# Optimization experiments

Hardware: AMD Instinct MI355X
Metric: run time of the kernel (lower is better)

## Reference

```python
import jax, jax.numpy as jnp
import numpy as np

B, N, D = 32768, 20, 13  # batch, n_humans, rotated-state dim (last input channel is mask)
LAYERS = {
    'm1': [(D, 150), (150, 100)],          # mlp1, last_relu=True
    'm2': [(100, 100), (100, 50)],          # mlp2
    'at': [(200, 100), (100, 100), (100, 1)],  # attention (global state concat -> 2*100 in)
    'hp': [(100, 100), (100, 100), (100, 7)],  # human_state_predictor (50*2 in)
}

def _mlp(x, params, last_relu=False):
    n = len(params)
    for i, (W, b) in enumerate(params):
        x = x @ W + b
        if i < n - 1 or last_relu:
            x = jax.nn.relu(x)
    return x

def setup_inputs() -> dict:
    key = jax.random.key(0)
    ks, kx, km = jax.random.split(key, 3)
    inp = {}
    for name, shapes in LAYERS.items():
        for i, (fi, fo) in enumerate(shapes):
            kw, kb, ks = jax.random.split(jax.random.fold_in(ks, i), 3)
            inp[f'{name}_w{i}'] = jax.random.normal(kw, (fi, fo), jnp.float32) / jnp.sqrt(float(fi))
            inp[f'{name}_b{i}'] = jnp.zeros((fo,), jnp.float32)
    x = jax.random.normal(kx, (B, N, D + 1), jnp.float32)
    mask = (jax.random.uniform(km, (B, N)) < 0.9).astype(jnp.float32)  # 0/1 visibility mask
    inp['state'] = x.at[..., -1].set(mask)
    return inp

def reference(state, m1_w0, m1_b0, m1_w1, m1_b1,
              m2_w0, m2_b0, m2_w1, m2_b1,
              at_w0, at_b0, at_w1, at_b1, at_w2, at_b2,
              hp_w0, hp_b0, hp_w1, hp_b1, hp_w2, hp_b2):
    x, mask = state[..., :-1], state[..., -1]        # (B,N,D), (B,N)
    h1 = _mlp(x, [(m1_w0, m1_b0), (m1_w1, m1_b1)], last_relu=True)   # (B,N,100)
    h2 = _mlp(h1, [(m2_w0, m2_b0), (m2_w1, m2_b1)])                   # (B,N,50)

    # masked mean-pool global state (NaN-on-empty zeroed, as in torch)
    msum = jnp.sum(mask, axis=1, keepdims=True)                       # (B,1)
    mw = jnp.where(msum > 0, mask / jnp.where(msum > 0, msum, 1.0), 0.0)
    global_state = jnp.sum(mw[..., None] * h1, axis=1, keepdims=True) # (B,1,100)
    att_in = jnp.concatenate([h1, jnp.broadcast_to(global_state, h1.shape)], axis=-1)

    scores = _mlp(att_in, [(at_w0, at_b0), (at_w1, at_b1), (at_w2, at_b2)])[..., 0]  # (B,N)
    scores = scores * mask
    se = jnp.exp(scores) * (scores != 0).astype(scores.dtype)
    ssum = jnp.sum(se, axis=1, keepdims=True)
    w = jnp.where(ssum > 0, se / jnp.where(ssum > 0, ssum, 1.0), 0.0)[..., None]  # (B,N,1)

    wsum = jnp.sum(w * h2, axis=1, keepdims=True)                     # (B,1,50)
    joint = jnp.concatenate([h2, jnp.broadcast_to(wsum, h2.shape)], axis=-1)  # (B,N,100)
    return _mlp(joint, [(hp_w0, hp_b0), (hp_w1, hp_b1), (hp_w2, hp_b2)])      # (B,N,7)
```

## Files before the change

### kernel.cpp

```cpp
#include <hip/hip_runtime.h>


typedef short sx8 __attribute__((ext_vector_type(8)));
typedef short sx4 __attribute__((ext_vector_type(4)));
typedef float fx4 __attribute__((ext_vector_type(4)));

#define TB   512
#define NW   8
#define NB   4
#define MTOK 80
#define MT   5
#define CHH  640
#define CHG  128

#define OFF_BUFT 0
#define OFF_BUFA 25600
#define OFF_BUFH 46080
#define OFF_BUFG 56320
#define OFF_BIAS 60416
#define OFF_GRC  63808
#define OFF_WRC  65408
#define OFF_SC   67008
#define OFF_MASK 67328
#define OFF_MSUM 67648
#define OFF_SSUM 67664
#define SMEM_BYTES 67680

#define B_M1B0 0
#define B_M1B1 152
#define B_M2B0 256
#define B_M2B1 360
#define B_ATB0 416
#define B_ATB1 520
#define B_HPB0 624
#define B_HPB1 728
#define B_HPB2 832

#define WS_M1W0  0
#define WS_M1W1  5120
#define WS_M2W0  23040
#define WS_M2W1  37376
#define WS_ATW0  45568
#define WS_ATW1  59904
#define WS_HPW0  74240
#define WS_HPW1  81408
#define WS_HPW2  95744
#define WS_ATW0H 97792
#define WS_HPW0H 112128

__device__ __forceinline__ short f2b(float f) {
    unsigned u = __builtin_bit_cast(unsigned, f);
    u += 0x7FFFu + ((u >> 16) & 1u);
    return (short)(u >> 16);
}
__device__ __forceinline__ float b2f(short h) {
    unsigned u = ((unsigned)(unsigned short)h) << 16;
    return __builtin_bit_cast(float, u);
}

__device__ __forceinline__ void stg(const float* __restrict__ W, int N,
                                    int KR, int KPAD, int NR, int Nsrc,
                                    short* dst, int gtid, int gsz) {
    int K8 = KPAD >> 3;
    for (int idx = gtid; idx < NR * K8; idx += gsz) {
        int k8 = idx / NR, nl = idx - k8 * NR;
        int k0 = k8 << 3;
        sx8 h;
        #pragma unroll
        for (int i = 0; i < 8; ++i) {
            int k = k0 + i;
            float v = (k < KR && nl < Nsrc) ? W[k * N + nl] : 0.f;
            h[i] = f2b(v);
        }
        *(sx8*)(dst + (k8 * NR + nl) * 8) = h;
    }
}

__global__ void stage_weights(
    const float* __restrict__ m1w0, const float* __restrict__ m1w1,
    const float* __restrict__ m2w0, const float* __restrict__ m2w1,
    const float* __restrict__ atw0, const float* __restrict__ atw1,
    const float* __restrict__ hpw0, const float* __restrict__ hpw1,
    const float* __restrict__ hpw2, short* __restrict__ ws)
{
    int gtid = blockIdx.x * blockDim.x + threadIdx.x;
    int gsz = gridDim.x * blockDim.x;
    stg(m1w0, 150, 13, 32, 160, 150, ws + WS_M1W0, gtid, gsz);
    stg(m1w1, 100, 150, 160, 112, 100, ws + WS_M1W1, gtid, gsz);
    stg(m2w0, 100, 100, 128, 112, 100, ws + WS_M2W0, gtid, gsz);
    stg(m2w1, 50, 100, 128, 64, 50, ws + WS_M2W1, gtid, gsz);
    stg(atw0, 100, 100, 128, 112, 100, ws + WS_ATW0, gtid, gsz);
    stg(atw1, 100, 100, 128, 112, 100, ws + WS_ATW1, gtid, gsz);
    stg(hpw0, 100, 50, 64, 112, 100, ws + WS_HPW0, gtid, gsz);
    stg(hpw1, 100, 100, 128, 112, 100, ws + WS_HPW1, gtid, gsz);
    stg(hpw2, 7, 100, 128, 16, 7, ws + WS_HPW2, gtid, gsz);
    stg(atw0 + 100 * 100, 100, 100, 128, 112, 100, ws + WS_ATW0H, gtid, gsz);
    stg(hpw0 + 50 * 100, 100, 50, 64, 112, 100, ws + WS_HPW0H, gtid, gsz);
}

template <int KT, int NT, bool RELU, bool UINIT>
__device__ __forceinline__ void gemm(const short* __restrict__ wg, int NR,
                                     const short* bIn, short* bOut,
                                     const float* initp, int initBstride,
                                     int Nreal, int wave, int lm, int lq) {
    constexpr int NG = (NT + 1) / 2;
    for (int u = wave; u < NG * 3; u += NW) {
        int ng = u / 3, mg = u - ng * 3;
        int nt0 = ng * 2, nt1 = nt0 + 1;
        bool hasN1 = !((NT & 1) && (ng == NG - 1));
        sx8 a0[KT], a1[KT];
        #pragma unroll
        for (int kt = 0; kt < KT; ++kt)
            a0[kt] = *(const sx8*)(wg + ((kt * 4 + lq) * NR + nt0 * 16 + lm) * 8);
        if (hasN1) {
            #pragma unroll
            for (int kt = 0; kt < KT; ++kt)
                a1[kt] = *(const sx8*)(wg + ((kt * 4 + lq) * NR + nt1 * 16 + lm) * 8);
        }
        int n0l0 = nt0 * 16 + lq * 4;
        int n0l1 = nt1 * 16 + lq * 4;
        fx4 ib0, ib1;
        if (UINIT) {
            ib0 = *(const fx4*)(initp + n0l0);
            if (hasN1) ib1 = *(const fx4*)(initp + n0l1);
        }
        int mcount = (mg == 2) ? 1 : 2;
        #pragma unroll 2
        for (int mi = 0; mi < mcount; ++mi) {
            int mt = mg * 2 + mi;
            int tok = mt * 16 + lm;
            sx8 bfr[KT];
            #pragma unroll
            for (int kt = 0; kt < KT; ++kt)
                bfr[kt] = *(const sx8*)(bIn + (kt * 4 + lq) * CHH + tok * 8);
            fx4 acc0, acc1;
            if (UINIT) acc0 = ib0;
            else acc0 = *(const fx4*)(initp + (tok / 20) * initBstride + n0l0);
            if (hasN1) {
                if (UINIT) acc1 = ib1;
                else acc1 = *(const fx4*)(initp + (tok / 20) * initBstride + n0l1);
            }
            #pragma unroll
            for (int kt = 0; kt < KT; ++kt) {
                acc0 = __builtin_amdgcn_mfma_f32_16x16x32_bf16(a0[kt], bfr[kt], acc0, 0, 0, 0);
                if (hasN1)
                    acc1 = __builtin_amdgcn_mfma_f32_16x16x32_bf16(a1[kt], bfr[kt], acc1, 0, 0, 0);
            }
            sx4 hv;
            #pragma unroll
            for (int r = 0; r < 4; ++r) {
                float v = acc0[r];
                if (RELU) v = fmaxf(v, 0.f);
                if (n0l0 + r >= Nreal) v = 0.f;
                hv[r] = f2b(v);
            }
            *(sx4*)(bOut + (nt0 * 2 + (lq >> 1)) * CHH + tok * 8 + (lq & 1) * 4) = hv;
            if (hasN1) {
                #pragma unroll
                for (int r = 0; r < 4; ++r) {
                    float v = acc1[r];
                    if (RELU) v = fmaxf(v, 0.f);
                    if (n0l1 + r >= Nreal) v = 0.f;
                    hv[r] = f2b(v);
                }
                *(sx4*)(bOut + (nt1 * 2 + (lq >> 1)) * CHH + tok * 8 + (lq & 1) * 4) = hv;
            }
        }
    }
}

template <int KT, int NT>
__device__ __forceinline__ void gemmR(const short* __restrict__ wg, int NR,
                                      const short* bG, float* outF,
                                      const float* biasp,
                                      int wave, int lm, int lq) {
    constexpr int NG = (NT + 1) / 2;
    for (int u = wave; u < NG; u += NW) {
        int nt0 = u * 2, nt1 = nt0 + 1;
        bool hasN1 = !((NT & 1) && (u == NG - 1));
        sx8 a0[KT], a1[KT], bfr[KT];
        #pragma unroll
        for (int kt = 0; kt < KT; ++kt) {
            a0[kt] = *(const sx8*)(wg + ((kt * 4 + lq) * NR + nt0 * 16 + lm) * 8);
            bfr[kt] = *(const sx8*)(bG + (kt * 4 + lq) * CHG + lm * 8);
        }
        if (hasN1) {
            #pragma unroll
            for (int kt = 0; kt < KT; ++kt)
                a1[kt] = *(const sx8*)(wg + ((kt * 4 + lq) * NR + nt1 * 16 + lm) * 8);
        }
        int n0l0 = nt0 * 16 + lq * 4;
        int n0l1 = nt1 * 16 + lq * 4;
        fx4 acc0 = *(const fx4*)(biasp + n0l0);
        fx4 acc1;
        if (hasN1) acc1 = *(const fx4*)(biasp + n0l1);
        #pragma unroll
        for (int kt = 0; kt < KT; ++kt) {
            acc0 = __builtin_amdgcn_mfma_f32_16x16x32_bf16(a0[kt], bfr[kt], acc0, 0, 0, 0);
            if (hasN1)
                acc1 = __builtin_amdgcn_mfma_f32_16x16x32_bf16(a1[kt], bfr[kt], acc1, 0, 0, 0);
        }
        if (lm < NB) {
            #pragma unroll
            for (int r = 0; r < 4; ++r) {
                int n = n0l0 + r;
                if (n < 100) outF[lm * 100 + n] = acc0[r];
            }
            if (hasN1) {
                #pragma unroll
                for (int r = 0; r < 4; ++r) {
                    int n = n0l1 + r;
                    if (n < 100) outF[lm * 100 + n] = acc1[r];
                }
            }
        }
    }
}

__device__ __forceinline__ void zpad(short* buf, int tid) {
    for (int i = tid; i < 160; i += TB) {
        sx8 z = {0, 0, 0, 0, 0, 0, 0, 0};
        *(sx8*)(buf + 14 * CHH + i * 8) = z;
    }
}

__global__ __launch_bounds__(TB, 4) void sp_mfma_bf16(
    const float* __restrict__ state,
    const float* __restrict__ m1b0, const float* __restrict__ m1b1,
    const float* __restrict__ m2b0, const float* __restrict__ m2b1,
    const float* __restrict__ atb0, const float* __restrict__ atb1,
    const float* __restrict__ atw2, const float* __restrict__ atb2,
    const float* __restrict__ hpb0, const float* __restrict__ hpb1,
    const float* __restrict__ hpb2,
    const short* __restrict__ ws,
    float* __restrict__ out)
{
    __shared__ __align__(16) unsigned char smem[SMEM_BYTES];
    short* bufT  = (short*)(smem + OFF_BUFT);
    short* bufA  = (short*)(smem + OFF_BUFA);
    short* bufH2 = (short*)(smem + OFF_BUFH);
    short* bufG  = (short*)(smem + OFF_BUFG);
    float* biasv = (float*)(smem + OFF_BIAS);
    float* grc   = (float*)(smem + OFF_GRC);
    float* wrc   = (float*)(smem + OFF_WRC);
    float* scv   = (float*)(smem + OFF_SC);
    float* maskv = (float*)(smem + OFF_MASK);
    float* msum  = (float*)(smem + OFF_MSUM);
    float* ssum  = (float*)(smem + OFF_SSUM);

    const int tid  = threadIdx.x;
    const int lane = tid & 63;
    const int wave = tid >> 6;
    const int lm   = lane & 15;
    const int lq   = lane >> 4;
    const long gt0 = (long)blockIdx.x * MTOK;

    {
        const float* bs[9] = {m1b0, m1b1, m2b0, m2b1, atb0, atb1, hpb0, hpb1, hpb2};
        const int off[9] = {B_M1B0, B_M1B1, B_M2B0, B_M2B1, B_ATB0, B_ATB1, B_HPB0, B_HPB1, B_HPB2};
        const int sz[9]  = {150, 100, 100, 50, 100, 100, 100, 100, 7};
        const int pd[9]  = {152, 104, 104, 56, 104, 104, 104, 104, 16};
        #pragma unroll
        for (int r = 0; r < 9; ++r)
            for (int i = tid; i < pd[r]; i += TB)
                biasv[off[r] + i] = (i < sz[r]) ? bs[r][i] : 0.f;
        if (tid < MTOK) maskv[tid] = state[(gt0 + tid) * 14 + 13];
        for (int idx = tid; idx < MTOK * 4; idx += TB) {
            int row = idx >> 2, seg = idx & 3;
            const float* xp = state + (gt0 + row) * 14;
            sx8 h;
            #pragma unroll
            for (int i = 0; i < 8; ++i) {
                int k = seg * 8 + i;
                float v = (k < 13) ? xp[k] : 0.f;
                h[i] = f2b(v);
            }
            *(sx8*)(bufA + seg * CHH + row * 8) = h;
        }
    }
    __syncthreads();

    if (tid < NB) {
        float s = 0.f;
        #pragma unroll
        for (int n = 0; n < 20; ++n) s += maskv[tid * 20 + n];
        msum[tid] = s;
    }
    gemm<1, 10, true, true>(ws + WS_M1W0, 160, bufA, bufT, biasv + B_M1B0, 0,
                            150, wave, lm, lq);
    __syncthreads();

    gemm<5, 7, true, true>(ws + WS_M1W1, 112, bufT, bufA, biasv + B_M1B1, 0,
                           100, wave, lm, lq);
    zpad(bufA, tid);
    __syncthreads();

    for (int t = tid; t < 2048; t += TB) {
        int c = t >> 7, rem = t & 127;
        int tg = rem >> 3, h = rem & 7;
        int j = c * 8 + h;
        float v = 0.f;
        if (tg < NB && j < 100) {
            float ms = msum[tg];
            float inv = (ms > 0.f) ? 1.f / ms : 0.f;
            float a = 0.f;
            #pragma unroll
            for (int n = 0; n < 20; ++n)
                a = fmaf(maskv[tg * 20 + n],
                         b2f(bufA[(j >> 3) * CHH + (tg * 20 + n) * 8 + (j & 7)]), a);
            v = a * inv;
        }
        bufG[t] = f2b(v);
    }
    __syncthreads();

    gemmR<4, 7>(ws + WS_ATW0H, 112, bufG, grc, biasv + B_ATB0, wave, lm, lq);
    gemm<4, 7, true, true>(ws + WS_M2W0, 112, bufA, bufT, biasv + B_M2B0, 0,
                           100, wave, lm, lq);
    zpad(bufT, tid);
    __syncthreads();

    gemm<4, 4, false, true>(ws + WS_M2W1, 64, bufT, bufH2, biasv + B_M2B1, 0,
                            50, wave, lm, lq);
    __syncthreads();

    gemm<4, 7, true, false>(ws + WS_ATW0, 112, bufA, bufT, grc, 100,
                            100, wave, lm, lq);
    __syncthreads();

    gemm<4, 7, true, true>(ws + WS_ATW1, 112, bufT, bufA, biasv + B_ATB1, 0,
                           100, wave, lm, lq);
    __syncthreads();

    if (tid < MTOK) {
        float s = atb2[0];
        #pragma unroll
        for (int k8 = 0; k8 < 13; ++k8) {
            sx8 v = *(const sx8*)(bufA + k8 * CHH + tid * 8);
            #pragma unroll
            for (int i = 0; i < 8; ++i) {
                int k = k8 * 8 + i;
                if (k < 100) s = fmaf(b2f(v[i]), atw2[k], s);
            }
        }
        s *= maskv[tid];
        scv[tid] = (s != 0.f) ? __expf(s) : 0.f;
    }
    __syncthreads();
    if (tid < NB) {
        float s = 0.f;
        #pragma unroll
        for (int n = 0; n < 20; ++n) s += scv[tid * 20 + n];
        ssum[tid] = s;
    }
    __syncthreads();

    for (int t = tid; t < 1024; t += TB) {
        int c = t >> 7, rem = t & 127;
        int tg = rem >> 3, h = rem & 7;
        int j = c * 8 + h;
        float v = 0.f;
        if (tg < NB && j < 50) {
            float ss = ssum[tg];
            float inv = (ss > 0.f) ? 1.f / ss : 0.f;
            float a = 0.f;
            #pragma unroll
            for (int n = 0; n < 20; ++n)
                a = fmaf(scv[tg * 20 + n],
                         b2f(bufH2[(j >> 3) * CHH + (tg * 20 + n) * 8 + (j & 7)]), a);
            v = a * inv;
        }
        bufG[t] = f2b(v);
    }
    __syncthreads();

    gemmR<2, 7>(ws + WS_HPW0H, 112, bufG, wrc, biasv + B_HPB0, wave, lm, lq);
    __syncthreads();

    gemm<2, 7, true, false>(ws + WS_HPW0, 112, bufH2, bufT, wrc, 100,
                            100, wave, lm, lq);
    __syncthreads();

    gemm<4, 7, true, true>(ws + WS_HPW1, 112, bufT, bufA, biasv + B_HPB1, 0,
                           100, wave, lm, lq);
    __syncthreads();

    {
        sx8 afr[4];
        #pragma unroll
        for (int kt = 0; kt < 4; ++kt)
            afr[kt] = *(const sx8*)(ws + WS_HPW2 + ((kt * 4 + lq) * 16 + lm) * 8);
        fx4 ib = *(const fx4*)(biasv + B_HPB2 + lq * 4);
        for (int mt = wave; mt < MT; mt += NW) {
            int tok = mt * 16 + lm;
            fx4 acc = ib;
            const short* bp = bufA + tok * 8;
            #pragma unroll
            for (int kt = 0; kt < 4; ++kt) {
                sx8 b = *(const sx8*)(bp + (kt * 4 + lq) * CHH);
                acc = __builtin_amdgcn_mfma_f32_16x16x32_bf16(afr[kt], b, acc, 0, 0, 0);
            }
            #pragma unroll
            for (int r = 0; r < 4; ++r) {
                int n = lq * 4 + r;
                if (n < 7) out[(gt0 + tok) * 7 + n] = acc[r];
            }
        }
    }
}

extern "C" void kernel_launch(void* const* d_in, const int* in_sizes, int n_in,
                              void* d_out, int out_size, void* d_ws, size_t ws_size,
                              hipStream_t stream) {
    int si = 20, wb = 0;
    if (in_sizes[0] > 1000000) { si = 0; wb = 1; }
    const float* state = (const float*)d_in[si];
    const float* W[20];
    for (int i = 0; i < 20; ++i) W[i] = (const float*)d_in[wb + i];
    float* out = (float*)d_out;
    short* ws = (short*)d_ws;
    int Btot = in_sizes[si] / (20 * 14);
    int nblocks = Btot / NB;

    hipLaunchKernelGGL(stage_weights, dim3(128), dim3(256), 0, stream,
        W[0], W[2], W[4], W[6], W[8], W[10], W[14], W[16], W[18], ws);

    hipLaunchKernelGGL(sp_mfma_bf16, dim3(nblocks), dim3(TB), 0, stream,
        state,
        W[1], W[3],
        W[5], W[7],
        W[9], W[11],
        W[12], W[13],
        W[15], W[17], W[19],
        ws, out);
}
```

Baseline: 453.5 us.

## Move pooling reductions and attention score projection onto MFMA

The masked-mean pooling and the softmax-weighted pooling, previously scalar 20-term FMA loops per feature, become small MFMA GEMMs against a per-block weight matrix built in LDS with a lane-rotated token layout. The attention score dot product (100->1) now uses an MFMA against a bf16-staged atw2 instead of 80 threads looping serially. The gemmR for the global state is moved after the next barrier and overlapped with the m2w1 GEMM, which removes one sync. The cost is about 3KB of extra LDS and bf16 rounding of the pooling weights and atw2, which may slightly change accuracy.

```diff
diff --git a/kernel.cpp b/kernel.cpp
--- a/kernel.cpp
+++ b/kernel.cpp
@@ -24,7 +24,8 @@
 #define OFF_MASK 67328
 #define OFF_MSUM 67648
 #define OFF_SSUM 67664
-#define SMEM_BYTES 67680
+#define OFF_WTM  67680
+#define SMEM_BYTES 70752
 
 #define B_M1B0 0
 #define B_M1B1 152
@@ -47,6 +48,7 @@
 #define WS_HPW2  95744
 #define WS_ATW0H 97792
 #define WS_HPW0H 112128
+#define WS_ATW2  119296
 
 __device__ __forceinline__ short f2b(float f) {
     unsigned u = __builtin_bit_cast(unsigned, f);
@@ -81,7 +83,8 @@
     const float* __restrict__ m2w0, const float* __restrict__ m2w1,
     const float* __restrict__ atw0, const float* __restrict__ atw1,
     const float* __restrict__ hpw0, const float* __restrict__ hpw1,
-    const float* __restrict__ hpw2, short* __restrict__ ws)
+    const float* __restrict__ hpw2, const float* __restrict__ atw2,
+    short* __restrict__ ws)
 {
     int gtid = blockIdx.x * blockDim.x + threadIdx.x;
     int gsz = gridDim.x * blockDim.x;
@@ -96,6 +99,7 @@
     stg(hpw2, 7, 100, 128, 16, 7, ws + WS_HPW2, gtid, gsz);
     stg(atw0 + 100 * 100, 100, 100, 128, 112, 100, ws + WS_ATW0H, gtid, gsz);
     stg(hpw0 + 50 * 100, 100, 50, 64, 112, 100, ws + WS_HPW0H, gtid, gsz);
+    stg(atw2, 1, 100, 128, 16, 1, ws + WS_ATW2, gtid, gsz);
 }
 
 template <int KT, int NT, bool RELU, bool UINIT>
@@ -217,6 +221,39 @@
     }
 }
 
+template <int NT, int NREAL>
+__device__ __forceinline__ void gemmT(const short* __restrict__ act,
+                                      const short* __restrict__ wT,
+                                      short* __restrict__ bG,
+                                      int wave, int lm, int lq) {
+    for (int nt = wave; nt < NT; nt += NW) {
+        int j = nt * 16 + lm;
+        const short* ap = act + (j >> 3) * CHH + (j & 7);
+        fx4 acc = {0.f, 0.f, 0.f, 0.f};
+        #pragma unroll
+        for (int kt = 0; kt < 3; ++kt) {
+            int tok0 = kt * 32 + lq * 8;
+            int tok0e = (tok0 < MTOK) ? tok0 : 0;
+            sx8 a;
+            #pragma unroll
+            for (int i = 0; i < 8; ++i) {
+                int ii = (i + lq * 2) & 7;
+                a[i] = ap[(tok0e + ii) * 8];
+            }
+            sx8 b = *(const sx8*)(wT + lm * 96 + tok0);
+            acc = __builtin_amdgcn_mfma_f32_16x16x32_bf16(a, b, acc, 0, 0, 0);
+        }
+        if (lm < NB) {
+            int j0 = nt * 16 + lq * 4;
+            sx4 hv;
+            #pragma unroll
+            for (int r = 0; r < 4; ++r)
+                hv[r] = f2b((j0 + r < NREAL) ? acc[r] : 0.f);
+            *(sx4*)(bG + (nt * 2 + (lq >> 1)) * CHG + lm * 8 + (lq & 1) * 4) = hv;
+        }
+    }
+}
+
 __device__ __forceinline__ void zpad(short* buf, int tid) {
     for (int i = tid; i < 160; i += TB) {
         sx8 z = {0, 0, 0, 0, 0, 0, 0, 0};
@@ -229,7 +266,7 @@
     const float* __restrict__ m1b0, const float* __restrict__ m1b1,
     const float* __restrict__ m2b0, const float* __restrict__ m2b1,
     const float* __restrict__ atb0, const float* __restrict__ atb1,
-    const float* __restrict__ atw2, const float* __restrict__ atb2,
+    const float* __restrict__ atb2,
     const float* __restrict__ hpb0, const float* __restrict__ hpb1,
     const float* __restrict__ hpb2,
     const short* __restrict__ ws,
@@ -246,7 +283,7 @@
     float* scv   = (float*)(smem + OFF_SC);
     float* maskv = (float*)(smem + OFF_MASK);
     float* msum  = (float*)(smem + OFF_MSUM);
-    float* ssum  = (float*)(smem + OFF_SSUM);
+    short* wTm   = (short*)(smem + OFF_WTM);
 
     const int tid  = threadIdx.x;
     const int lane = tid & 63;
@@ -265,6 +302,10 @@
             for (int i = tid; i < pd[r]; i += TB)
                 biasv[off[r] + i] = (i < sz[r]) ? bs[r][i] : 0.f;
         if (tid < MTOK) maskv[tid] = state[(gt0 + tid) * 14 + 13];
+        for (int t = tid; t < 256; t += TB) {
+            sx8 z = {0, 0, 0, 0, 0, 0, 0, 0};
+            *(sx8*)(bufG + t * 8) = z;
+        }
         for (int idx = tid; idx < MTOK * 4; idx += TB) {
             int row = idx >> 2, seg = idx & 3;
             const float* xp = state + (gt0 + row) * 14;
@@ -293,33 +334,25 @@
     gemm<5, 7, true, true>(ws + WS_M1W1, 112, bufT, bufA, biasv + B_M1B1, 0,
                            100, wave, lm, lq);
     zpad(bufA, tid);
-    __syncthreads();
-
-    for (int t = tid; t < 2048; t += TB) {
-        int c = t >> 7, rem = t & 127;
-        int tg = rem >> 3, h = rem & 7;
-        int j = c * 8 + h;
+    for (int t = tid; t < 1536; t += TB) {
+        int b = t / 96, tp = t - b * 96;
+        int tau = (tp & ~7) | ((tp + ((tp >> 3) & 3) * 2) & 7);
         float v = 0.f;
-        if (tg < NB && j < 100) {
-            float ms = msum[tg];
-            float inv = (ms > 0.f) ? 1.f / ms : 0.f;
-            float a = 0.f;
-            #pragma unroll
-            for (int n = 0; n < 20; ++n)
-                a = fmaf(maskv[tg * 20 + n],
-                         b2f(bufA[(j >> 3) * CHH + (tg * 20 + n) * 8 + (j & 7)]), a);
-            v = a * inv;
-        }
-        bufG[t] = f2b(v);
-    }
-    __syncthreads();
-
-    gemmR<4, 7>(ws + WS_ATW0H, 112, bufG, grc, biasv + B_ATB0, wave, lm, lq);
+        if (b < NB && tau < MTOK && tau / 20 == b) {
+            float ms = msum[b];
+            v = (ms > 0.f) ? maskv[tau] / ms : 0.f;
+        }
+        wTm[t] = f2b(v);
+    }
+    __syncthreads();
+
+    gemmT<7, 100>(bufA, wTm, bufG, wave, lm, lq);
     gemm<4, 7, true, true>(ws + WS_M2W0, 112, bufA, bufT, biasv + B_M2B0, 0,
                            100, wave, lm, lq);
     zpad(bufT, tid);
     __syncthreads();
 
+    gemmR<4, 7>(ws + WS_ATW0H, 112, bufG, grc, biasv + B_ATB0, wave, lm, lq);
     gemm<4, 4, false, true>(ws + WS_M2W1, 64, bufT, bufH2, biasv + B_M2B1, 0,
                             50, wave, lm, lq);
     __syncthreads();
@@ -332,46 +365,44 @@
                            100, wave, lm, lq);
     __syncthreads();
 
-    if (tid < MTOK) {
-        float s = atb2[0];
-        #pragma unroll
-        for (int k8 = 0; k8 < 13; ++k8) {
-            sx8 v = *(const sx8*)(bufA + k8 * CHH + tid * 8);
-            #pragma unroll
-            for (int i = 0; i < 8; ++i) {
-                int k = k8 * 8 + i;
-                if (k < 100) s = fmaf(b2f(v[i]), atw2[k], s);
-            }
-        }
-        s *= maskv[tid];
-        scv[tid] = (s != 0.f) ? __expf(s) : 0.f;
-    }
-    __syncthreads();
-    if (tid < NB) {
-        float s = 0.f;
-        #pragma unroll
-        for (int n = 0; n < 20; ++n) s += scv[tid * 20 + n];
-        ssum[tid] = s;
-    }
-    __syncthreads();
-
-    for (int t = tid; t < 1024; t += TB) {
-        int c = t >> 7, rem = t & 127;
-        int tg = rem >> 3, h = rem & 7;
-        int j = c * 8 + h;
+    {
+        float atb2s = atb2[0];
+        sx8 afr[4];
+        #pragma unroll
+        for (int kt = 0; kt < 4; ++kt)
+            afr[kt] = *(const sx8*)(ws + WS_ATW2 + ((kt * 4 + lq) * 16 + lm) * 8);
+        for (int mt = wave; mt < MT; mt += NW) {
+            int tok = mt * 16 + lm;
+            fx4 acc = {0.f, 0.f, 0.f, 0.f};
+            const short* bp = bufA + tok * 8;
+            #pragma unroll
+            for (int kt = 0; kt < 4; ++kt) {
+                sx8 b = *(const sx8*)(bp + (kt * 4 + lq) * CHH);
+                acc = __builtin_amdgcn_mfma_f32_16x16x32_bf16(afr[kt], b, acc, 0, 0, 0);
+            }
+            if (lq == 0) {
+                float s = (acc[0] + atb2s) * maskv[tok];
+                scv[tok] = (s != 0.f) ? __expf(s) : 0.f;
+            }
+        }
+    }
+    __syncthreads();
+
+    for (int t = tid; t < 1536; t += TB) {
+        int b = t / 96, tp = t - b * 96;
+        int tau = (tp & ~7) | ((tp + ((tp >> 3) & 3) * 2) & 7);
         float v = 0.f;
-        if (tg < NB && j < 50) {
-            float ss = ssum[tg];
-            float inv = (ss > 0.f) ? 1.f / ss : 0.f;
-            float a = 0.f;
-            #pragma unroll
-            for (int n = 0; n < 20; ++n)
-                a = fmaf(scv[tg * 20 + n],
-                         b2f(bufH2[(j >> 3) * CHH + (tg * 20 + n) * 8 + (j & 7)]), a);
-            v = a * inv;
-        }
-        bufG[t] = f2b(v);
-    }
+        if (b < NB && tau < MTOK && tau / 20 == b) {
+            float ss = 0.f;
+            #pragma unroll
+            for (int n = 0; n < 20; ++n) ss += scv[b * 20 + n];
+            v = (ss > 0.f) ? scv[tau] / ss : 0.f;
+        }
+        wTm[t] = f2b(v);
+    }
+    __syncthreads();
+
+    gemmT<4, 50>(bufH2, wTm, bufG, wave, lm, lq);
     __syncthreads();
 
     gemmR<2, 7>(ws + WS_HPW0H, 112, bufG, wrc, biasv + B_HPB0, wave, lm, lq);
@@ -423,14 +454,14 @@
     int nblocks = Btot / NB;
 
     hipLaunchKernelGGL(stage_weights, dim3(128), dim3(256), 0, stream,
-        W[0], W[2], W[4], W[6], W[8], W[10], W[14], W[16], W[18], ws);
+        W[0], W[2], W[4], W[6], W[8], W[10], W[14], W[16], W[18], W[12], ws);
 
     hipLaunchKernelGGL(sp_mfma_bf16, dim3(nblocks), dim3(TB), 0, stream,
         state,
         W[1], W[3],
         W[5], W[7],
         W[9], W[11],
-        W[12], W[13],
+        W[13],
         W[15], W[17], W[19],
         ws, out);
 }
```

Result: faster. 430.2 us (-5.1%).
